# Optimization experiments

Hardware: AMD Instinct MI355X
Metric: run time of the kernel (lower is better)

The kernel has to match this reference:

```python
import jax, jax.numpy as jnp
import numpy as np

B, T, V = 128, 35, 10000
F, E, H = 1408, 512, 512
R = 81  # 9x9 regions for EfficientNet-b2


def setup_inputs() -> dict:
    key = jax.random.key(0)
    ks = jax.random.split(key, 16)
    s = 0.02
    return {
        "image_features": jax.random.normal(ks[0], (B, R, F), jnp.float32),
        "input_seqs": jax.random.randint(ks[1], (B, T), 0, V),
        "lengths": jax.random.randint(ks[2], (B,), 1, T),
        "emb": jax.random.normal(ks[3], (V, E), jnp.float32) * s,
        "W_ih": jax.random.normal(ks[4], (4 * H, E + F), jnp.float32) * s,
        "b_ih": jnp.zeros((4 * H,), jnp.float32),
        "W_hh": jax.random.normal(ks[5], (4 * H, H), jnp.float32) * s,
        "b_hh": jnp.zeros((4 * H,), jnp.float32),
        "W_init_h": jax.random.normal(ks[6], (H, F), jnp.float32) * s,
        "b_init_h": jnp.zeros((H,), jnp.float32),
        "W_init_c": jax.random.normal(ks[7], (H, F), jnp.float32) * s,
        "b_init_c": jnp.zeros((H,), jnp.float32),
        "W_fc1": jax.random.normal(ks[8], (H, H), jnp.float32) * s,
        "b_fc1": jnp.zeros((H,), jnp.float32),
        "W_fc2": jax.random.normal(ks[9], (V, H), jnp.float32) * s,
        "b_fc2": jnp.zeros((V,), jnp.float32),
    }


def reference(image_features, input_seqs, lengths, emb, W_ih, b_ih, W_hh, b_hh,
              W_init_h, b_init_h, W_init_c, b_init_c, W_fc1, b_fc1, W_fc2, b_fc2):
    # dropout layers are identity in eval mode
    mean_feats = image_features.mean(axis=1)                 # (B, F)
    h0 = jnp.tanh(mean_feats @ W_init_h.T + b_init_h)        # (B, H)
    c0 = jnp.tanh(mean_feats @ W_init_c.T + b_init_c)        # (B, H)
    emb_seq = emb[input_seqs]                                # (B, T, E)
    # precompute input-side gate contributions for all steps (no recurrence needed)
    x_seq = jnp.concatenate(
        [emb_seq, jnp.broadcast_to(mean_feats[:, None, :], (emb_seq.shape[0], emb_seq.shape[1], mean_feats.shape[1]))],
        axis=2)                                              # (B, T, E+F)
    gx_seq = jnp.einsum('bte,ge->btg', x_seq, W_ih) + b_ih + b_hh  # (B, T, 4H)

    def step(carry, gx_t):
        h, c = carry
        gates = gx_t + h @ W_hh.T                            # (B, 4H)
        i, f, g, o = jnp.split(gates, 4, axis=1)
        i, f, o = jax.nn.sigmoid(i), jax.nn.sigmoid(f), jax.nn.sigmoid(o)
        g = jnp.tanh(g)
        c = f * c + i * g
        h = o * jnp.tanh(c)
        out = jax.nn.relu(h @ W_fc1.T + b_fc1)
        logits = out @ W_fc2.T + b_fc2                       # (B, V)
        return (h, c), logits

    _, logits_t = jax.lax.scan(step, (h0, c0), gx_seq.transpose(1, 0, 2))
    return logits_t.transpose(1, 0, 2)                       # (B, T, V)
```

## Files before the change

kernel.cpp:

```cpp
#include <hip/hip_runtime.h>

#define TB 35
#define BB 128
#define VV 10000
#define FF 1408
#define EE 512
#define HH 512
#define G4 2048
#define NBLK 32

typedef unsigned short u16;
typedef unsigned long long u64;
typedef __attribute__((ext_vector_type(8))) short bfrag;
typedef __attribute__((ext_vector_type(4))) float f32x4;

__device__ __forceinline__ u16 f2bf(float f) {
    unsigned u = __float_as_uint(f);
    return (u16)((u + 0x7FFFu + ((u >> 16) & 1u)) >> 16);
}
__device__ __forceinline__ float fast_sig(float x) {
    return __builtin_amdgcn_rcpf(1.f + __expf(-x));
}
__device__ __forceinline__ float fast_tanh(float x) {
    return 1.f - 2.f * __builtin_amdgcn_rcpf(1.f + __expf(2.f * x));
}

__device__ __forceinline__ void gload16(const void* g, void* l) {
    __builtin_amdgcn_global_load_lds(
        (const __attribute__((address_space(1))) void*)g,
        (__attribute__((address_space(3))) void*)l, 16, 0, 0);
}

__global__ __launch_bounds__(256)
void mean_k(const float* __restrict__ img, float* __restrict__ mf) {
    int idx = blockIdx.x * 256 + threadIdx.x;
    int b = idx / FF, f = idx - b * FF;
    const float* p = img + (long)b * (81 * FF) + f;
    float s = 0.f;
    for (int r = 0; r < 81; ++r) s += p[r * FF];
    mf[idx] = s * (1.f / 81.f);
}

__global__ __launch_bounds__(256)
void cast512_k(const float* __restrict__ src, int lds, u16* __restrict__ dst, int n4) {
    int i = blockIdx.x * 256 + threadIdx.x;
    if (i >= n4) return;
    long e = (long)i * 4;
    long row = e >> 9; int col = (int)(e & 511);
    float4 v = *(const float4*)(src + row * lds + col);
    uint2 o;
    o.x = (unsigned)f2bf(v.x) | ((unsigned)f2bf(v.y) << 16);
    o.y = (unsigned)f2bf(v.z) | ((unsigned)f2bf(v.w) << 16);
    *(uint2*)(dst + e) = o;
}

__global__ __launch_bounds__(256)
void init_partial_k(const float* __restrict__ mf,
                    const float* __restrict__ Wh, const float* __restrict__ Wc,
                    const float* __restrict__ Wih,
                    float* __restrict__ part)
{
    __shared__ float As[16][68];
    __shared__ float Ws[16][68];
    const int t  = threadIdx.x;
    const int bx = blockIdx.x;
    const int bm = blockIdx.y * 64;
    const int kz = blockIdx.z;
    const float* W; int ldw; long wr0;
    if (bx < 8)       { W = Wh;       ldw = FF;   wr0 = (long)bx * 64; }
    else if (bx < 16) { W = Wc;       ldw = FF;   wr0 = (long)(bx - 8) * 64; }
    else              { W = Wih + EE; ldw = 1920; wr0 = (long)(bx - 16) * 64; }
    const int lrow = t >> 2, lc4 = (t & 3) << 2;
    const int ty = t >> 4, tx = t & 15;
    const float* arow = mf + (long)(bm + lrow) * FF;
    const float* wrow = W + (wr0 + lrow) * (long)ldw;
    float acc[4][4] = {};
    const int kbeg = kz * 352, kend2 = kbeg + 352;
    for (int k0 = kbeg; k0 < kend2; k0 += 16) {
        float4 av = *(const float4*)(arow + k0 + lc4);
        float4 wv = *(const float4*)(wrow + k0 + lc4);
        As[lc4+0][lrow]=av.x; As[lc4+1][lrow]=av.y; As[lc4+2][lrow]=av.z; As[lc4+3][lrow]=av.w;
        Ws[lc4+0][lrow]=wv.x; Ws[lc4+1][lrow]=wv.y; Ws[lc4+2][lrow]=wv.z; Ws[lc4+3][lrow]=wv.w;
        __syncthreads();
        #pragma unroll
        for (int kk = 0; kk < 16; ++kk) {
            float4 a = *(const float4*)&As[kk][ty*4];
            float4 w = *(const float4*)&Ws[kk][tx*4];
            acc[0][0]+=a.x*w.x; acc[0][1]+=a.x*w.y; acc[0][2]+=a.x*w.z; acc[0][3]+=a.x*w.w;
            acc[1][0]+=a.y*w.x; acc[1][1]+=a.y*w.y; acc[1][2]+=a.y*w.z; acc[1][3]+=a.y*w.w;
            acc[2][0]+=a.z*w.x; acc[2][1]+=a.z*w.y; acc[2][2]+=a.z*w.z; acc[2][3]+=a.z*w.w;
            acc[3][0]+=a.w*w.x; acc[3][1]+=a.w*w.y; acc[3][2]+=a.w*w.z; acc[3][3]+=a.w*w.w;
        }
        __syncthreads();
    }
    const int ncol = bx * 64;
    #pragma unroll
    for (int i = 0; i < 4; ++i) {
        long base = (long)kz * (BB*3072) + (long)(bm + ty*4 + i) * 3072 + ncol + tx*4;
        *(float4*)(part + base) = make_float4(acc[i][0], acc[i][1], acc[i][2], acc[i][3]);
    }
}

__global__ __launch_bounds__(256)
void init_combine_k(const float* __restrict__ part,
                    const float* __restrict__ b_ih, const float* __restrict__ b_hh,
                    const float* __restrict__ b_init_h, const float* __restrict__ b_init_c,
                    u16* __restrict__ h0b, float* __restrict__ c_cur, float* __restrict__ gxb,
                    unsigned* __restrict__ bar)
{
    int idx = blockIdx.x * 256 + threadIdx.x;
    if (idx < 1024) bar[idx] = 0;
    int b = idx / 3072, n = idx - b * 3072;
    float s = part[idx] + part[393216 + idx] + part[2*393216 + idx] + part[3*393216 + idx];
    if (n < 512)       h0b[b*512 + n]         = f2bf(tanhf(s + b_init_h[n]));
    else if (n < 1024) c_cur[b*512 + (n-512)] = tanhf(s + b_init_c[n-512]);
    else               gxb[b*2048 + (n-1024)] = s + b_ih[n-1024] + b_hh[n-1024];
}

template<int ACT, int OBF>
__global__ __launch_bounds__(256)
void gemm_mfma(const u16* __restrict__ A, int lda, const int* __restrict__ rowidx,
               const u16* __restrict__ W, const float* __restrict__ bias,
               const float* __restrict__ radd, int radd_div, int radd_ld,
               void* __restrict__ C, int cdiv, long csq, long csr,
               int mtiles, int N, int K)
{
    __shared__ u16 lA[4096];
    __shared__ u16 lB[4096];
    int bxi, byi;
    if (mtiles > 0) {
        int nwg = gridDim.x, bid = blockIdx.x;
        int q = nwg >> 3, r = nwg & 7;
        int xcd = bid & 7, pos = bid >> 3;
        int lid = (xcd < r) ? (xcd * (q + 1) + pos)
                            : (r * (q + 1) + (xcd - r) * q + pos);
        byi = lid % mtiles;
        bxi = lid / mtiles;
    } else { bxi = blockIdx.x; byi = blockIdx.y; }

    const int t    = threadIdx.x;
    const int bm   = byi * 128;
    const int bn   = bxi * 128;
    const int lane = t & 63;
    const int wv   = t >> 6;
    const int wm   = (wv >> 1) * 64;
    const int wn   = (wv & 1) * 64;
    const int fr   = lane & 15;
    const int cc   = lane >> 4;

    const int q0 = t, q1 = t + 256;
    const int ra0 = q0 >> 2, ca0 = (q0 & 3) ^ ((ra0 >> 1) & 3);
    const int ra1 = q1 >> 2, ca1 = (q1 & 3) ^ ((ra1 >> 1) & 3);
    long arow0 = rowidx ? (long)rowidx[bm + ra0] : (long)(bm + ra0);
    long arow1 = rowidx ? (long)rowidx[bm + ra1] : (long)(bm + ra1);
    const u16* asrc0 = A + arow0 * lda + ca0 * 8;
    const u16* asrc1 = A + arow1 * lda + ca1 * 8;
    int brow0 = bn + ra0; if (brow0 > N - 1) brow0 = N - 1;
    int brow1 = bn + ra1; if (brow1 > N - 1) brow1 = N - 1;
    const u16* bsrc0 = W + (long)brow0 * K + ca0 * 8;
    const u16* bsrc1 = W + (long)brow1 * K + ca1 * 8;
    u16* adst0 = lA + q0 * 8;  u16* adst1 = lA + q1 * 8;
    u16* bdst0 = lB + q0 * 8;  u16* bdst1 = lB + q1 * 8;

    int aoff[4], boff[4];
    #pragma unroll
    for (int i = 0; i < 4; ++i) {
        int rA = wm + i * 16 + fr;
        aoff[i] = rA * 64 + ((cc ^ ((rA >> 1) & 3)) << 4);
        int rB = wn + i * 16 + fr;
        boff[i] = rB * 64 + ((cc ^ ((rB >> 1) & 3)) << 4);
    }
    const char* lac = (const char*)lA;
    const char* lbc = (const char*)lB;

    f32x4 acc[4][4] = {};
    for (int k0 = 0; k0 < K; k0 += 32) {
        gload16(asrc0 + k0, adst0);
        gload16(asrc1 + k0, adst1);
        gload16(bsrc0 + k0, bdst0);
        gload16(bsrc1 + k0, bdst1);
        __syncthreads();
        bfrag av[4], bv[4];
        #pragma unroll
        for (int i = 0; i < 4; ++i) av[i] = *(const bfrag*)(lac + aoff[i]);
        #pragma unroll
        for (int i = 0; i < 4; ++i) bv[i] = *(const bfrag*)(lbc + boff[i]);
        #pragma unroll
        for (int mi = 0; mi < 4; ++mi)
            #pragma unroll
            for (int ni = 0; ni < 4; ++ni)
                acc[mi][ni] = __builtin_amdgcn_mfma_f32_16x16x32_bf16(
                    av[mi], bv[ni], acc[mi][ni], 0, 0, 0);
        __syncthreads();
    }

    #pragma unroll
    for (int mi = 0; mi < 4; ++mi) {
        #pragma unroll
        for (int r = 0; r < 4; ++r) {
            int m = bm + wm + mi * 16 + (lane >> 4) * 4 + r;
            long cb = (long)(m / cdiv) * csq + (long)(m % cdiv) * csr;
            const float* rr = radd ? (radd + (long)(m / radd_div) * radd_ld) : nullptr;
            #pragma unroll
            for (int ni = 0; ni < 4; ++ni) {
                int n = bn + wn + ni * 16 + fr;
                if (n < N) {
                    float v = acc[mi][ni][r];
                    if (bias) v += bias[n];
                    if (rr)   v += rr[n];
                    if (ACT == 2) v = fmaxf(v, 0.f);
                    if (OBF) ((u16*)C)[cb + n] = f2bf(v);
                    else     ((float*)C)[cb + n] = v;
                }
            }
        }
    }
}

template<int ACT, int OBF>
__device__ __forceinline__ void tile_gemm(u16* shm, const u16* Abase, const u16* W,
                                          int bn, int N, const float* bias,
                                          char* Cbase, long crs )
{
    u16* lA = shm;
    u16* lB = shm + 4096;
    const int t    = threadIdx.x;
    const int lane = t & 63;
    const int wv   = t >> 6;
    const int wm   = (wv >> 1) * 64;
    const int wn   = (wv & 1) * 64;
    const int fr   = lane & 15;
    const int cc   = lane >> 4;

    const int q0 = t, q1 = t + 256;
    const int ra0 = q0 >> 2, ca0 = (q0 & 3) ^ ((ra0 >> 1) & 3);
    const int ra1 = q1 >> 2, ca1 = (q1 & 3) ^ ((ra1 >> 1) & 3);
    const u16* asrc0 = Abase + (long)ra0 * 512 + ca0 * 8;
    const u16* asrc1 = Abase + (long)ra1 * 512 + ca1 * 8;
    int brow0 = bn + ra0; if (brow0 > N - 1) brow0 = N - 1;
    int brow1 = bn + ra1; if (brow1 > N - 1) brow1 = N - 1;
    const u16* bsrc0 = W + (long)brow0 * 512 + ca0 * 8;
    const u16* bsrc1 = W + (long)brow1 * 512 + ca1 * 8;
    u16* adst0 = lA + q0 * 8;  u16* adst1 = lA + q1 * 8;
    u16* bdst0 = lB + q0 * 8;  u16* bdst1 = lB + q1 * 8;

    int aoff[4], boff[4];
    #pragma unroll
    for (int i = 0; i < 4; ++i) {
        int rA = wm + i * 16 + fr;
        aoff[i] = rA * 64 + ((cc ^ ((rA >> 1) & 3)) << 4);
        int rB = wn + i * 16 + fr;
        boff[i] = 8192 + rB * 64 + ((cc ^ ((rB >> 1) & 3)) << 4);
    }
    const char* lc = (const char*)lA;

    f32x4 acc[4][4] = {};
    for (int k0 = 0; k0 < 512; k0 += 32) {
        gload16(asrc0 + k0, adst0);
        gload16(asrc1 + k0, adst1);
        gload16(bsrc0 + k0, bdst0);
        gload16(bsrc1 + k0, bdst1);
        __syncthreads();
        bfrag av[4], bv[4];
        #pragma unroll
        for (int i = 0; i < 4; ++i) av[i] = *(const bfrag*)(lc + aoff[i]);
        #pragma unroll
        for (int i = 0; i < 4; ++i) bv[i] = *(const bfrag*)(lc + boff[i]);
        #pragma unroll
        for (int mi = 0; mi < 4; ++mi)
            #pragma unroll
            for (int ni = 0; ni < 4; ++ni)
                acc[mi][ni] = __builtin_amdgcn_mfma_f32_16x16x32_bf16(
                    av[mi], bv[ni], acc[mi][ni], 0, 0, 0);
        __syncthreads();
    }

    #pragma unroll
    for (int mi = 0; mi < 4; ++mi) {
        #pragma unroll
        for (int r = 0; r < 4; ++r) {
            int m = wm + mi * 16 + (lane >> 4) * 4 + r;
            char* crow = Cbase + (long)m * crs;
            #pragma unroll
            for (int ni = 0; ni < 4; ++ni) {
                int n = bn + wn + ni * 16 + fr;
                if (n < N) {
                    float v = acc[mi][ni][r] + bias[n];
                    if (ACT == 2) v = fmaxf(v, 0.f);
                    if (OBF)
                        __hip_atomic_store((u16*)crow + n, f2bf(v),
                                           __ATOMIC_RELAXED, __HIP_MEMORY_SCOPE_AGENT);
                    else
                        __builtin_nontemporal_store(v, (float*)crow + n);
                }
            }
        }
    }
}

__global__ __launch_bounds__(256, 1)
void mega_k(const u16* __restrict__ h0b, const float* __restrict__ c0,
            const float* __restrict__ Whh, const float* __restrict__ gx,
            u16* __restrict__ h_b, unsigned* __restrict__ bar,
            const u16* __restrict__ wfc1, const float* __restrict__ b_fc1,
            u16* __restrict__ o_b,
            const u16* __restrict__ wfc2, const float* __restrict__ b_fc2,
            float* __restrict__ out)
{
    __shared__ alignas(16) u16 shm[32768];
    const int bid  = blockIdx.x;
    const int t256 = threadIdx.x;
    const int lane = t256 & 63;

    if (bid < NBLK) {
        bfrag* Wf = (bfrag*)shm;
        const int jb = bid;
        const int w  = t256 >> 6;
        const int fr = lane & 15;
        const int cc = lane >> 4;

        for (int q = 0; q < 16; ++q) {
            int flat = t256 + q * 256;
            int r = flat >> 6, kg = flat & 63;
            int mi = r >> 4, jj = r & 15;
            int kk = kg >> 2, c2 = kg & 3;
            const float* src = Whh + (long)(mi * 512 + jb * 16 + jj) * 512 + kg * 8;
            float4 s0 = *(const float4*)src;
            float4 s1 = *(const float4*)(src + 4);
            bfrag p;
            p[0] = (short)f2bf(s0.x); p[1] = (short)f2bf(s0.y);
            p[2] = (short)f2bf(s0.z); p[3] = (short)f2bf(s0.w);
            p[4] = (short)f2bf(s1.x); p[5] = (short)f2bf(s1.y);
            p[6] = (short)f2bf(s1.z); p[7] = (short)f2bf(s1.w);
            Wf[(kk * 4 + mi) * 64 + c2 * 16 + jj] = p;
        }

        const int b0   = w * 32 + fr;
        const int jcol = jb * 16 + cc * 4;

        f32x4 creg[2];
        #pragma unroll
        for (int ni = 0; ni < 2; ++ni)
            creg[ni] = *(const f32x4*)(c0 + (long)(b0 + ni*16) * 512 + jcol);

        f32x4 gxc[4][2];
        #pragma unroll
        for (int ni = 0; ni < 2; ++ni) {
            const float* gp = gx + (long)(b0 + ni*16) * G4 + jcol;
            #pragma unroll
            for (int g = 0; g < 4; ++g) gxc[g][ni] = *(const f32x4*)(gp + g * 512);
        }

        __syncthreads();

        const u16* hsrc = h0b;
        for (int t = 0; t < TB; ++t) {
            bfrag hreg[2][16];
            #pragma unroll
            for (int ni = 0; ni < 2; ++ni) {
                const u16* hp = hsrc + (long)(b0 + ni*16) * 512 + cc * 8;
                #pragma unroll
                for (int kk = 0; kk < 16; ++kk)
                    hreg[ni][kk] = *(const bfrag*)(hp + kk * 32);
            }

            f32x4 acc[4][2] = {};
            #pragma unroll
            for (int kk = 0; kk < 16; ++kk) {
                bfrag av0 = Wf[(kk*4 + 0) * 64 + lane];
                bfrag av1 = Wf[(kk*4 + 1) * 64 + lane];
                bfrag av2 = Wf[(kk*4 + 2) * 64 + lane];
                bfrag av3 = Wf[(kk*4 + 3) * 64 + lane];
                #pragma unroll
                for (int ni = 0; ni < 2; ++ni) {
                    acc[0][ni] = __builtin_amdgcn_mfma_f32_16x16x32_bf16(av0, hreg[ni][kk], acc[0][ni], 0,0,0);
                    acc[1][ni] = __builtin_amdgcn_mfma_f32_16x16x32_bf16(av1, hreg[ni][kk], acc[1][ni], 0,0,0);
                    acc[2][ni] = __builtin_amdgcn_mfma_f32_16x16x32_bf16(av2, hreg[ni][kk], acc[2][ni], 0,0,0);
                    acc[3][ni] = __builtin_amdgcn_mfma_f32_16x16x32_bf16(av3, hreg[ni][kk], acc[3][ni], 0,0,0);
                }
            }

            u16* hd = h_b + (long)t * (BB*HH);
            #pragma unroll
            for (int ni = 0; ni < 2; ++ni) {
                u64 hq = 0;
                #pragma unroll
                for (int rr = 0; rr < 4; ++rr) {
                    float ig = fast_sig (acc[0][ni][rr] + gxc[0][ni][rr]);
                    float fg = fast_sig (acc[1][ni][rr] + gxc[1][ni][rr]);
                    float gg = fast_tanh(acc[2][ni][rr] + gxc[2][ni][rr]);
                    float og = fast_sig (acc[3][ni][rr] + gxc[3][ni][rr]);
                    float c  = fg * creg[ni][rr] + ig * gg;
                    creg[ni][rr] = c;
                    hq |= (u64)f2bf(og * fast_tanh(c)) << (rr * 16);
                }
                __hip_atomic_store((u64*)(hd + (long)(b0 + ni*16) * 512 + jcol), hq,
                                   __ATOMIC_RELAXED, __HIP_MEMORY_SCOPE_AGENT);
            }
            hsrc = hd;

            if (t < TB - 1) {
                f32x4 gxn[4][2];
                #pragma unroll
                for (int ni = 0; ni < 2; ++ni) {
                    const float* gp = gx + ((long)(t+1) * BB + b0 + ni*16) * G4 + jcol;
                    #pragma unroll
                    for (int g = 0; g < 4; ++g) gxn[g][ni] = *(const f32x4*)(gp + g * 512);
                }
                __syncthreads();
                if (t256 < 64) {
                    if (lane == 0)
                        __hip_atomic_store(&bar[jb], (unsigned)(t + 1),
                                           __ATOMIC_RELAXED, __HIP_MEMORY_SCOPE_AGENT);
                    while (true) {
                        unsigned v = __hip_atomic_load(&bar[lane & 31],
                                                       __ATOMIC_RELAXED, __HIP_MEMORY_SCOPE_AGENT);
                        if (__all(v > (unsigned)t)) break;
                        __builtin_amdgcn_s_sleep(1);
                    }
                }
                __syncthreads();
                __builtin_amdgcn_fence(__ATOMIC_ACQUIRE, "agent");
                #pragma unroll
                for (int g = 0; g < 4; ++g)
                    #pragma unroll
                    for (int ni = 0; ni < 2; ++ni) gxc[g][ni] = gxn[g][ni];
            } else {
                __syncthreads();
                if (t256 == 0)
                    __hip_atomic_store(&bar[jb], (unsigned)TB,
                                       __ATOMIC_RELAXED, __HIP_MEMORY_SCOPE_AGENT);
            }
        }
    } else if (bid < 64) {
        const int wkr = bid - 32;
        for (int g = wkr; g < TB * 4; g += 32) {
            int tt = g >> 2, nt4 = g & 3;
            if (t256 < 64) {
                while (true) {
                    unsigned v = __hip_atomic_load(&bar[lane & 31],
                                                   __ATOMIC_RELAXED, __HIP_MEMORY_SCOPE_AGENT);
                    if (__all(v > (unsigned)tt)) break;
                    __builtin_amdgcn_s_sleep(8);
                }
            }
            __syncthreads();
            __builtin_amdgcn_fence(__ATOMIC_ACQUIRE, "agent");
            tile_gemm<2,1>(shm, h_b + (long)tt * (BB*HH), wfc1, nt4 * 128, HH, b_fc1,
                           (char*)(o_b + (long)tt * (BB*HH)), HH * 2);
            __syncthreads();
            if (t256 == 0)
                __hip_atomic_fetch_add(bar + 600 + tt, 1u,
                                       __ATOMIC_RELAXED, __HIP_MEMORY_SCOPE_AGENT);
        }
    } else {
        const int wkr = bid - 64;
        for (int g = wkr; g < TB * 79; g += 192) {
            int tt = g / 79, nt = g - tt * 79;
            if (t256 == 0) {
                while (__hip_atomic_load(bar + 600 + tt, __ATOMIC_RELAXED,
                                         __HIP_MEMORY_SCOPE_AGENT) < 4)
                    __builtin_amdgcn_s_sleep(8);
            }
            __syncthreads();
            __builtin_amdgcn_fence(__ATOMIC_ACQUIRE, "agent");
            tile_gemm<0,0>(shm, o_b + (long)tt * (BB*HH), wfc2, nt * 128, VV, b_fc2,
                           (char*)(out + (long)tt * VV), (long)TB * VV * 4);
        }
    }
}

extern "C" void kernel_launch(void* const* d_in, const int* in_sizes, int n_in,
                              void* d_out, int out_size, void* d_ws, size_t ws_size,
                              hipStream_t stream)
{
    const float* img    = (const float*)d_in[0];
    const int*   seqs   = (const int*)d_in[1];
    const float* emb    = (const float*)d_in[3];
    const float* W_ih   = (const float*)d_in[4];
    const float* b_ih   = (const float*)d_in[5];
    const float* W_hh   = (const float*)d_in[6];
    const float* b_hh   = (const float*)d_in[7];
    const float* W_inh  = (const float*)d_in[8];
    const float* b_inh  = (const float*)d_in[9];
    const float* W_inc  = (const float*)d_in[10];
    const float* b_inc  = (const float*)d_in[11];
    const float* W_fc1  = (const float*)d_in[12];
    const float* b_fc1  = (const float*)d_in[13];
    const float* W_fc2  = (const float*)d_in[14];
    const float* b_fc2  = (const float*)d_in[15];
    float* out = (float*)d_out;

    float*    ws  = (float*)d_ws;
    unsigned* bar = (unsigned*)ws;
    float* mf    = ws    + 1024;
    float* c_cur = mf    + 180224;
    float* gxb   = c_cur + 65536;
    float* gx    = gxb   + 262144;
    float* ipart = gx;
    u16*   h_b    = (u16*)(gx + 9175040);
    u16*   h0b    = h_b    + 2293760;
    u16*   emb_b  = h0b    + 65536;
    u16*   wih_b  = emb_b  + 5120000;
    u16*   wfc1_b = wih_b  + 1048576;
    u16*   wfc2_b = wfc1_b + 262144;
    u16*   o_b    = wfc2_b + 5120000;

    cast512_k<<<5000, 256, 0, stream>>>(emb,   512,  emb_b,  1280000);
    cast512_k<<<1024, 256, 0, stream>>>(W_ih,  1920, wih_b,   262144);
    cast512_k<<< 256, 256, 0, stream>>>(W_fc1, 512,  wfc1_b,   65536);
    cast512_k<<<5000, 256, 0, stream>>>(W_fc2, 512,  wfc2_b, 1280000);

    mean_k<<<704, 256, 0, stream>>>(img, mf);
    init_partial_k<<<dim3(48, 2, 4), 256, 0, stream>>>(mf, W_inh, W_inc, W_ih, ipart);
    init_combine_k<<<1536, 256, 0, stream>>>(ipart, b_ih, b_hh, b_inh, b_inc,
                                             h0b, c_cur, gxb, bar);

    gemm_mfma<0,0><<<dim3(16 * 35), 256, 0, stream>>>(emb_b, EE, seqs, wih_b, nullptr,
                                                      gxb, TB, G4, gx, TB, G4,
                                                      (long)BB * G4, 35, G4, EE);

    mega_k<<<dim3(256), dim3(256), 0, stream>>>(h0b, c_cur, W_hh, gx, h_b, bar,
                                                wfc1_b, b_fc1, o_b, wfc2_b, b_fc2, out);
}
```

Baseline: 485.9 us.

## Use per-wave barrier flags in LSTM recurrence and fuse prologue cast kernels

Replaces the block-wide __syncthreads plus single flag per block in the recurrent loop with per-wave flags: each wave publishes its own progress and spins only on the 32 flags for its batch slice, so waves advance independently. The next step's gx prefetch is moved before the MFMA loop to overlap its latency. The four weight-cast kernels and the mean kernel are merged into one launch to cut launch overhead. Consumers of h now poll two flag ranges, and correctness relies on the vmcnt wait and acquire fence ordering the h stores correctly.

```diff
diff --git a/kernel.cpp b/kernel.cpp
--- a/kernel.cpp
+++ b/kernel.cpp
@@ -31,27 +31,37 @@
         (__attribute__((address_space(3))) void*)l, 16, 0, 0);
 }
 
-__global__ __launch_bounds__(256)
-void mean_k(const float* __restrict__ img, float* __restrict__ mf) {
-    int idx = blockIdx.x * 256 + threadIdx.x;
-    int b = idx / FF, f = idx - b * FF;
-    const float* p = img + (long)b * (81 * FF) + f;
-    float s = 0.f;
-    for (int r = 0; r < 81; ++r) s += p[r * FF];
-    mf[idx] = s * (1.f / 81.f);
-}
-
-__global__ __launch_bounds__(256)
-void cast512_k(const float* __restrict__ src, int lds, u16* __restrict__ dst, int n4) {
-    int i = blockIdx.x * 256 + threadIdx.x;
-    if (i >= n4) return;
-    long e = (long)i * 4;
+__device__ __forceinline__ void cast4(const float* __restrict__ src, int lds,
+                                      u16* __restrict__ dst, long i) {
+    long e = i * 4;
     long row = e >> 9; int col = (int)(e & 511);
     float4 v = *(const float4*)(src + row * lds + col);
     uint2 o;
     o.x = (unsigned)f2bf(v.x) | ((unsigned)f2bf(v.y) << 16);
     o.y = (unsigned)f2bf(v.z) | ((unsigned)f2bf(v.w) << 16);
     *(uint2*)(dst + e) = o;
+}
+
+__global__ __launch_bounds__(256)
+void prolog_k(const float* __restrict__ emb, const float* __restrict__ W_ih,
+              const float* __restrict__ W_fc1, const float* __restrict__ W_fc2,
+              u16* __restrict__ emb_b, u16* __restrict__ wih_b,
+              u16* __restrict__ wfc1_b, u16* __restrict__ wfc2_b,
+              const float* __restrict__ img, float* __restrict__ mf)
+{
+    long i = (long)blockIdx.x * 256 + threadIdx.x;
+    if (i < 1280000)      cast4(emb,   512,  emb_b,  i);
+    else if (i < 1542144) cast4(W_ih,  1920, wih_b,  i - 1280000);
+    else if (i < 1607680) cast4(W_fc1, 512,  wfc1_b, i - 1542144);
+    else if (i < 2887680) cast4(W_fc2, 512,  wfc2_b, i - 1607680);
+    else if (i < 3067904) {
+        int idx = (int)(i - 2887680);
+        int b = idx / FF, f = idx - b * FF;
+        const float* p = img + (long)b * (81 * FF) + f;
+        float s = 0.f;
+        for (int r = 0; r < 81; ++r) s += p[r * FF];
+        mf[idx] = s * (1.f / 81.f);
+    }
 }
 
 __global__ __launch_bounds__(256)
@@ -335,8 +345,9 @@
             Wf[(kk * 4 + mi) * 64 + c2 * 16 + jj] = p;
         }
 
-        const int b0   = w * 32 + fr;
-        const int jcol = jb * 16 + cc * 4;
+        const int b0    = w * 32 + fr;
+        const int jcol  = jb * 16 + cc * 4;
+        unsigned* fl    = bar + w * 32;
 
         f32x4 creg[2];
         #pragma unroll
@@ -362,6 +373,15 @@
                 #pragma unroll
                 for (int kk = 0; kk < 16; ++kk)
                     hreg[ni][kk] = *(const bfrag*)(hp + kk * 32);
+            }
+            f32x4 gxn[4][2];
+            if (t < TB - 1) {
+                #pragma unroll
+                for (int ni = 0; ni < 2; ++ni) {
+                    const float* gp = gx + ((long)(t+1) * BB + b0 + ni*16) * G4 + jcol;
+                    #pragma unroll
+                    for (int g = 0; g < 4; ++g) gxn[g][ni] = *(const f32x4*)(gp + g * 512);
+                }
             }
 
             f32x4 acc[4][2] = {};
@@ -399,37 +419,23 @@
             }
             hsrc = hd;
 
+            asm volatile("s_waitcnt vmcnt(0)" ::: "memory");
+            __builtin_amdgcn_sched_barrier(0);
+            if (lane == 0)
+                __hip_atomic_store(&fl[jb], (unsigned)(t + 1),
+                                   __ATOMIC_RELAXED, __HIP_MEMORY_SCOPE_AGENT);
             if (t < TB - 1) {
-                f32x4 gxn[4][2];
-                #pragma unroll
-                for (int ni = 0; ni < 2; ++ni) {
-                    const float* gp = gx + ((long)(t+1) * BB + b0 + ni*16) * G4 + jcol;
-                    #pragma unroll
-                    for (int g = 0; g < 4; ++g) gxn[g][ni] = *(const f32x4*)(gp + g * 512);
-                }
-                __syncthreads();
-                if (t256 < 64) {
-                    if (lane == 0)
-                        __hip_atomic_store(&bar[jb], (unsigned)(t + 1),
-                                           __ATOMIC_RELAXED, __HIP_MEMORY_SCOPE_AGENT);
-                    while (true) {
-                        unsigned v = __hip_atomic_load(&bar[lane & 31],
-                                                       __ATOMIC_RELAXED, __HIP_MEMORY_SCOPE_AGENT);
-                        if (__all(v > (unsigned)t)) break;
-                        __builtin_amdgcn_s_sleep(1);
-                    }
-                }
-                __syncthreads();
+                while (true) {
+                    unsigned v = __hip_atomic_load(&fl[lane & 31],
+                                                   __ATOMIC_RELAXED, __HIP_MEMORY_SCOPE_AGENT);
+                    if (__all(v > (unsigned)t)) break;
+                    __builtin_amdgcn_s_sleep(1);
+                }
                 __builtin_amdgcn_fence(__ATOMIC_ACQUIRE, "agent");
                 #pragma unroll
                 for (int g = 0; g < 4; ++g)
                     #pragma unroll
                     for (int ni = 0; ni < 2; ++ni) gxc[g][ni] = gxn[g][ni];
-            } else {
-                __syncthreads();
-                if (t256 == 0)
-                    __hip_atomic_store(&bar[jb], (unsigned)TB,
-                                       __ATOMIC_RELAXED, __HIP_MEMORY_SCOPE_AGENT);
             }
         }
     } else if (bid < 64) {
@@ -438,9 +444,11 @@
             int tt = g >> 2, nt4 = g & 3;
             if (t256 < 64) {
                 while (true) {
-                    unsigned v = __hip_atomic_load(&bar[lane & 31],
-                                                   __ATOMIC_RELAXED, __HIP_MEMORY_SCOPE_AGENT);
-                    if (__all(v > (unsigned)tt)) break;
+                    unsigned v0 = __hip_atomic_load(&bar[lane],
+                                                    __ATOMIC_RELAXED, __HIP_MEMORY_SCOPE_AGENT);
+                    unsigned v1 = __hip_atomic_load(&bar[64 + lane],
+                                                    __ATOMIC_RELAXED, __HIP_MEMORY_SCOPE_AGENT);
+                    if (__all((v0 > (unsigned)tt) && (v1 > (unsigned)tt))) break;
                     __builtin_amdgcn_s_sleep(8);
                 }
             }
@@ -506,12 +514,9 @@
     u16*   wfc2_b = wfc1_b + 262144;
     u16*   o_b    = wfc2_b + 5120000;
 
-    cast512_k<<<5000, 256, 0, stream>>>(emb,   512,  emb_b,  1280000);
-    cast512_k<<<1024, 256, 0, stream>>>(W_ih,  1920, wih_b,   262144);
-    cast512_k<<< 256, 256, 0, stream>>>(W_fc1, 512,  wfc1_b,   65536);
-    cast512_k<<<5000, 256, 0, stream>>>(W_fc2, 512,  wfc2_b, 1280000);
-
-    mean_k<<<704, 256, 0, stream>>>(img, mf);
+    prolog_k<<<11984, 256, 0, stream>>>(emb, W_ih, W_fc1, W_fc2,
+                                        emb_b, wih_b, wfc1_b, wfc2_b, img, mf);
+
     init_partial_k<<<dim3(48, 2, 4), 256, 0, stream>>>(mf, W_inh, W_inc, W_ih, ipart);
     init_combine_k<<<1536, 256, 0, stream>>>(ipart, b_ih, b_hh, b_inh, b_inc,
                                              h0b, c_cur, gxb, bar);
```

Measured after the change: 481.6 us (median of 2 runs). Within noise of the previous version (-0.9%).
